# Performance work log

Measured on AMD Instinct MI355X. Metric: run time of the kernel, lower is better.

## Reference

```python
import jax, jax.numpy as jnp
import numpy as np


def _rope_cos_sin(seq_len, dim, dtype):
    inv_freq = 1.0 / (10000.0 ** (jnp.arange(0, dim, 2, dtype=jnp.float32) / dim))
    t = jnp.arange(seq_len, dtype=jnp.float32)
    freqs = jnp.einsum('i,j->ij', t, inv_freq)          # [S, dim/2]
    emb = jnp.concatenate([freqs, freqs], axis=-1)       # [S, dim]
    return emb.astype(dtype).__class__ and (jnp.cos(emb).astype(dtype), jnp.sin(emb).astype(dtype))


def _apply_rope(x, cos, sin):
    half = x.shape[-1] // 2
    rot = jnp.concatenate([-x[..., half:], x[..., :half]], axis=-1)
    return x * cos + rot * sin


def setup_inputs() -> dict:
    key = jax.random.key(0)
    kq, kk, kv = jax.random.split(key, 3)
    B, S, D = 8, 4096, 128
    Q = jax.random.normal(kq, (B, S, D), dtype=jnp.float32)
    K = jax.random.normal(kk, (B, S, D), dtype=jnp.float32)
    V = jax.random.normal(kv, (B, S, D), dtype=jnp.float32)
    return {"Q": Q, "K": K, "V": V}


def reference(Q, K, V):
    B, S, D = Q.shape
    cos, sin = _rope_cos_sin(S, D, Q.dtype)              # [S, D] each
    Qr = _apply_rope(Q, cos, sin)
    Kr = _apply_rope(K, cos, sin)
    energy = jnp.einsum('bsd,btd->bst', Qr, Kr)          # [B, S, S]
    causal = jnp.tril(jnp.ones((S, S), dtype=bool))
    energy = jnp.where(causal, energy, jnp.zeros((), dtype=energy.dtype))
    return jnp.einsum('bst,btd->bsd', energy, V)
```

## Files before the change

### kernel.cpp

```cpp
#include <hip/hip_runtime.h>
#include <hip/hip_bf16.h>

#define B_ 8
#define S_ 4096
#define D_ 128
#define C_ 256
#define NC 16

typedef __attribute__((ext_vector_type(8))) short bf16x8;
typedef __attribute__((ext_vector_type(4))) float f32x4;
typedef __attribute__((ext_vector_type(4))) unsigned u32x4;

static __device__ __forceinline__ unsigned short f2bf(float x) {
    unsigned u = __float_as_uint(x);
    u += 0x7fffu + ((u >> 16) & 1u);
    return (unsigned short)(u >> 16);
}

typedef const __attribute__((address_space(1))) unsigned int* gas_ptr;
typedef __attribute__((address_space(3))) unsigned int* las_ptr;
static __device__ __forceinline__ void load_lds16(const unsigned short* g, unsigned short* l) {
    __builtin_amdgcn_global_load_lds((gas_ptr)(const void*)g, (las_ptr)(void*)l, 16, 0, 0);
}

#define WAIT_VMCNT_8 do { asm volatile("s_waitcnt vmcnt(8)" ::: "memory"); \
                          __builtin_amdgcn_sched_barrier(0); } while (0)
#define WAIT_VMCNT_0 do { asm volatile("s_waitcnt vmcnt(0)" ::: "memory"); \
                          __builtin_amdgcn_sched_barrier(0); } while (0)
#define BARRIER      do { __builtin_amdgcn_s_barrier(); \
                          __builtin_amdgcn_sched_barrier(0); } while (0)

__global__ __launch_bounds__(512, 2) void fusedA(const float* __restrict__ K,
                                                 const float* __restrict__ V,
                                                 unsigned short* __restrict__ Kr,
                                                 unsigned short* __restrict__ Vt,
                                                 float* __restrict__ P1) {
    __shared__ unsigned short Klds[128 * 128];
    __shared__ unsigned short Vlds[128 * 128];

    const int b    = blockIdx.x >> 5;
    const int c    = (blockIdx.x >> 1) & 15;
    const int half = blockIdx.x & 1;
    const int tid  = threadIdx.x;
    const int t0   = c * C_ + half * 128;

    #pragma unroll
    for (int it = 0; it < 4; ++it) {
        int e  = it * 512 + tid;
        int tl = e >> 4;
        int d0 = (e & 15) * 4;
        size_t gbase = ((size_t)(b * S_ + t0 + tl)) * D_;
        float ka[4], kb[4], va[4], vb[4];
        *(float4*)ka = *(const float4*)(K + gbase + d0);
        *(float4*)kb = *(const float4*)(K + gbase + d0 + 64);
        *(float4*)va = *(const float4*)(V + gbase + d0);
        *(float4*)vb = *(const float4*)(V + gbase + d0 + 64);
        unsigned short kl[4], kh[4];
        #pragma unroll
        for (int jj = 0; jj < 4; ++jj) {
            float invf = exp2f(-0.20762050f * (float)(d0 + jj));
            float ang = (float)(t0 + tl) * invf;
            float sn, cs;
            __sincosf(ang, &sn, &cs);
            kl[jj] = f2bf(ka[jj] * cs - kb[jj] * sn);
            kh[jj] = f2bf(kb[jj] * cs + ka[jj] * sn);
        }
        *reinterpret_cast<ushort4*>(Kr + gbase + d0)      = ushort4{kl[0], kl[1], kl[2], kl[3]};
        *reinterpret_cast<ushort4*>(Kr + gbase + d0 + 64) = ushort4{kh[0], kh[1], kh[2], kh[3]};
        int cc = tl >> 3, tr = tl & 7;
        #pragma unroll
        for (int jj = 0; jj < 4; ++jj) {
            int dA = d0 + jj, dB = d0 + 64 + jj;
            Klds[dA * 128 + ((cc ^ (dA & 15)) * 8) + tr] = kl[jj];
            Klds[dB * 128 + ((cc ^ (dB & 15)) * 8) + tr] = kh[jj];
            Vlds[dA * 128 + ((cc ^ (dA & 15)) * 8) + tr] = f2bf(va[jj]);
            Vlds[dB * 128 + ((cc ^ (dB & 15)) * 8) + tr] = f2bf(vb[jj]);
        }
    }
    __syncthreads();

    #pragma unroll
    for (int it = 0; it < 4; ++it) {
        int e = it * 512 + tid;
        int d = e >> 4;
        int cc = e & 15;
        const bf16x8 v8 = *reinterpret_cast<const bf16x8*>(
            &Vlds[d * 128 + ((cc ^ (d & 15)) * 8)]);
        *reinterpret_cast<bf16x8*>(
            Vt + ((size_t)(b * D_ + d)) * S_ + t0 + cc * 8) = v8;
    }

    const int w = tid >> 6, l = tid & 63, g = l >> 4, n = l & 15;
    f32x4 acc[8];
    #pragma unroll
    for (int dc = 0; dc < 8; ++dc) acc[dc] = f32x4{0.f, 0.f, 0.f, 0.f};

    #pragma unroll
    for (int ki = 0; ki < 4; ++ki) {
        const int arow = 16 * w + n;
        const bf16x8 a = *reinterpret_cast<const bf16x8*>(
            &Vlds[arow * 128 + (((4 * ki + g) ^ n) * 8)]);
        #pragma unroll
        for (int dc = 0; dc < 8; ++dc) {
            int row = dc * 16 + n;
            const bf16x8 bb = *reinterpret_cast<const bf16x8*>(
                &Klds[row * 128 + (((4 * ki + g) ^ n) * 8)]);
            acc[dc] = __builtin_amdgcn_mfma_f32_16x16x32_bf16(a, bb, acc[dc], 0, 0, 0);
        }
    }

    float* out = P1 + (size_t)((b * NC + c) * 2 + half) * D_ * D_;
    #pragma unroll
    for (int dc = 0; dc < 8; ++dc)
        #pragma unroll
        for (int rr = 0; rr < 4; ++rr)
            out[(size_t)(16 * w + 4 * g + rr) * D_ + dc * 16 + n] = acc[dc][rr];
}

__global__ __launch_bounds__(256) void prefix(const float* __restrict__ P1,
                                              unsigned short* __restrict__ Hhi) {
    int gid = blockIdx.x * 256 + threadIdx.x;
    int d  = gid & 127;
    int dp = (gid >> 7) & 127;
    int b  = gid >> 14;
    float run = 0.f;
    #pragma unroll
    for (int c = 0; c < NC; ++c) {
        size_t hidx = ((size_t)(b * NC + c) * D_ + dp) * D_ + d;
        Hhi[hidx] = f2bf(run);
        size_t p = ((size_t)((b * NC + c) * 2) * D_ + dp) * D_ + d;
        run += P1[p];
        run += P1[p + (size_t)D_ * D_];
    }
}

__global__ __launch_bounds__(256, 2) void pass2(const float* __restrict__ Q,
                                                const unsigned short* __restrict__ Kr,
                                                const unsigned short* __restrict__ Vt,
                                                const unsigned short* __restrict__ Hhi,
                                                float* __restrict__ Out) {
    __shared__ unsigned short Kb[2][64 * 128];
    __shared__ unsigned short Vb[2][128 * 64];

    const int bid = blockIdx.x;
    const int ppmap[4] = {3, 2, 0, 1};
    const int pp = ppmap[bid >> 7];
    const int r2 = bid & 127;
    const int b  = r2 & 7;
    const int c  = r2 >> 3;
    const int qg = c * 4 + pp;
    const int c4 = c * 4;

    const int tid = threadIdx.x;
    const int wv = tid >> 6;
    const int l  = tid & 63;
    const int g  = l >> 4;
    const int n  = l & 15;

    bf16x8 qf[4];
    {
        const int s = qg * 64 + wv * 16 + n;
        const float* qp = Q + ((size_t)(b * S_ + s)) * D_ + 8 * g;
        float qv[4][8];
        #pragma unroll
        for (int ks = 0; ks < 4; ++ks) {
            *reinterpret_cast<float4*>(&qv[ks][0]) =
                *reinterpret_cast<const float4*>(qp + 32 * ks);
            *reinterpret_cast<float4*>(&qv[ks][4]) =
                *reinterpret_cast<const float4*>(qp + 32 * ks + 4);
        }
        unsigned short qb[4][8];
        #pragma unroll
        for (int hf = 0; hf < 2; ++hf)
            #pragma unroll
            for (int j = 0; j < 8; ++j) {
                int dm = 32 * hf + 8 * g + j;
                float invf = exp2f(-0.20762050f * (float)dm);
                float ang = (float)s * invf;
                float sn, cs;
                __sincosf(ang, &sn, &cs);
                qb[hf][j]     = f2bf(qv[hf][j] * cs - qv[hf + 2][j] * sn);
                qb[hf + 2][j] = f2bf(qv[hf + 2][j] * cs + qv[hf][j] * sn);
            }
        #pragma unroll
        for (int ks = 0; ks < 4; ++ks) {
            bf16x8 f;
            #pragma unroll
            for (int j = 0; j < 8; ++j) f[j] = (short)qb[ks][j];
            qf[ks] = f;
        }
    }

    auto stage = [&](int bufs, int tg) {
        const unsigned short* kbase = Kr + ((size_t)(b * S_ + tg * 64)) * D_;
        #pragma unroll
        for (int i = 0; i < 4; ++i) {
            int ci = i * 256 + tid;
            int t = ci >> 4, cc = ci & 15;
            load_lds16(kbase + t * D_ + ((cc ^ (t & 15)) * 8), &Kb[bufs][ci * 8]);
        }
        const unsigned short* vbase = Vt + (size_t)b * D_ * S_ + (size_t)tg * 64;
        #pragma unroll
        for (int i = 0; i < 4; ++i) {
            int ci = i * 256 + tid;
            int d = ci >> 3, cc = ci & 7;
            load_lds16(vbase + (size_t)d * S_ + ((cc ^ (d & 7)) * 8), &Vb[bufs][ci * 8]);
        }
    };

    f32x4 o[8];
    #pragma unroll
    for (int df = 0; df < 8; ++df) o[df] = f32x4{0.f, 0.f, 0.f, 0.f};

    stage(0, c4);
    if (pp >= 1) stage(1, c4 + 1);

    {
        const unsigned short* hbase = Hhi + (size_t)(b * NC + c) * D_ * D_;
        #pragma unroll
        for (int ks = 0; ks < 4; ++ks) {
            #pragma unroll
            for (int df = 0; df < 8; ++df) {
                const bf16x8 hh = *reinterpret_cast<const bf16x8*>(
                    hbase + (size_t)(df * 16 + n) * D_ + 32 * ks + 8 * g);
                o[df] = __builtin_amdgcn_mfma_f32_16x16x32_bf16(qf[ks], hh, o[df], 0, 0, 0);
            }
        }
    }

    for (int kt = 0; kt <= pp; ++kt) {
        if (kt < pp) { WAIT_VMCNT_8; }
        else         { WAIT_VMCNT_0; }
        BARRIER;

        const int bufc = kt & 1;

        f32x4 e[4];
        #pragma unroll
        for (int tf = 0; tf < 4; ++tf) e[tf] = f32x4{0.f, 0.f, 0.f, 0.f};
        __builtin_amdgcn_s_setprio(1);
        #pragma unroll
        for (int tf = 0; tf < 4; ++tf) {
            #pragma unroll
            for (int ks = 0; ks < 4; ++ks) {
                const bf16x8 kf = *reinterpret_cast<const bf16x8*>(
                    &Kb[bufc][(tf * 16 + n) * 128 + (((4 * ks + g) ^ n) * 8)]);
                e[tf] = __builtin_amdgcn_mfma_f32_16x16x32_bf16(kf, qf[ks], e[tf], 0, 0, 0);
            }
        }
        __builtin_amdgcn_s_setprio(0);

        if (kt == pp) {
            int s_glob = qg * 64 + wv * 16 + n;
            #pragma unroll
            for (int tf = 0; tf < 4; ++tf)
                #pragma unroll
                for (int rr = 0; rr < 4; ++rr) {
                    int t_glob = (c4 + kt) * 64 + tf * 16 + 4 * g + rr;
                    if (t_glob > s_glob) e[tf][rr] = 0.f;
                }
        }

        bf16x8 pf[2];
        {
            unsigned u0[4], u1[4];
            #pragma unroll
            for (int tf = 0; tf < 4; ++tf) {
                asm("v_cvt_pk_bf16_f32 %0, %1, %2"
                    : "=v"(u0[tf]) : "v"(e[tf][0]), "v"(e[tf][1]));
                asm("v_cvt_pk_bf16_f32 %0, %1, %2"
                    : "=v"(u1[tf]) : "v"(e[tf][2]), "v"(e[tf][3]));
            }
            #pragma unroll
            for (int ks = 0; ks < 2; ++ks) {
                unsigned a0 = u0[2 * ks], a1 = u0[2 * ks + 1];
                unsigned b0 = u1[2 * ks], b1 = u1[2 * ks + 1];
                asm("v_permlane32_swap_b32 %0, %1" : "+v"(a0), "+v"(a1));
                asm("v_permlane32_swap_b32 %0, %1" : "+v"(b0), "+v"(b1));
                asm("v_permlane16_swap_b32 %0, %1" : "+v"(a0), "+v"(a1));
                asm("v_permlane16_swap_b32 %0, %1" : "+v"(b0), "+v"(b1));
                pf[ks] = __builtin_bit_cast(bf16x8, u32x4{a0, b0, a1, b1});
            }
        }

        __builtin_amdgcn_s_setprio(1);
        #pragma unroll
        for (int df = 0; df < 8; ++df) {
            #pragma unroll
            for (int ks = 0; ks < 2; ++ks) {
                const bf16x8 vf = *reinterpret_cast<const bf16x8*>(
                    &Vb[bufc][(df * 16 + n) * 64 + (((4 * ks + g) ^ (n & 7)) * 8)]);
                o[df] = __builtin_amdgcn_mfma_f32_16x16x32_bf16(pf[ks], vf, o[df], 0, 0, 0);
            }
        }
        __builtin_amdgcn_s_setprio(0);

        BARRIER;

        if (kt + 2 <= pp) stage(bufc, c4 + kt + 2);
    }

    #pragma unroll
    for (int df = 0; df < 8; ++df)
        #pragma unroll
        for (int rr = 0; rr < 4; ++rr) {
            int srow = qg * 64 + wv * 16 + 4 * g + rr;
            Out[((size_t)(b * S_ + srow)) * D_ + df * 16 + n] = o[df][rr];
        }
}

extern "C" void kernel_launch(void* const* d_in, const int* in_sizes, int n_in,
                              void* d_out, int out_size, void* d_ws, size_t ws_size,
                              hipStream_t stream) {
    const float* Q = (const float*)d_in[0];
    const float* K = (const float*)d_in[1];
    const float* V = (const float*)d_in[2];

    const size_t NE = (size_t)B_ * S_ * D_;
    unsigned short* Kr = (unsigned short*)d_ws;
    unsigned short* Vt = Kr + NE;
    float*          P1 = (float*)(Vt + NE);
    unsigned short* Hhi = (unsigned short*)(P1 + (size_t)B_ * NC * 2 * D_ * D_);

    fusedA<<<256, 512, 0, stream>>>(K, V, Kr, Vt, P1);
    prefix<<<512, 256, 0, stream>>>(P1, Hhi);
    pass2 <<<512, 256, 0, stream>>>(Q, Kr, Vt, Hhi, (float*)d_out);
}
```

Before: 40.74 us.

## Store partial KV products in bf16 and merge pass2 into 512-thread blocks

fusedA now writes its per-chunk K^T V partial products as bf16 instead of fp32, which halves the write and read traffic for the prefix kernel at the cost of extra rounding error. pass2 is restructured so each 512-thread block handles 128 query rows (8 waves), sharing the staged K/V tiles across twice as many waves and halving the grid. The staging loads are split over more threads and the wait count is adjusted to match. The causal mask is now applied on every tile iteration rather than only the last one, adding some ALU work, and each half-block now walks through 2 or 4 K tiles.

```diff
diff --git a/kernel.cpp b/kernel.cpp
--- a/kernel.cpp
+++ b/kernel.cpp
@@ -16,6 +16,9 @@
     u += 0x7fffu + ((u >> 16) & 1u);
     return (unsigned short)(u >> 16);
 }
+static __device__ __forceinline__ float bf2f(unsigned short h) {
+    return __uint_as_float(((unsigned)h) << 16);
+}
 
 typedef const __attribute__((address_space(1))) unsigned int* gas_ptr;
 typedef __attribute__((address_space(3))) unsigned int* las_ptr;
@@ -23,7 +26,7 @@
     __builtin_amdgcn_global_load_lds((gas_ptr)(const void*)g, (las_ptr)(void*)l, 16, 0, 0);
 }
 
-#define WAIT_VMCNT_8 do { asm volatile("s_waitcnt vmcnt(8)" ::: "memory"); \
+#define WAIT_VMCNT_4 do { asm volatile("s_waitcnt vmcnt(4)" ::: "memory"); \
                           __builtin_amdgcn_sched_barrier(0); } while (0)
 #define WAIT_VMCNT_0 do { asm volatile("s_waitcnt vmcnt(0)" ::: "memory"); \
                           __builtin_amdgcn_sched_barrier(0); } while (0)
@@ -34,7 +37,7 @@
                                                  const float* __restrict__ V,
                                                  unsigned short* __restrict__ Kr,
                                                  unsigned short* __restrict__ Vt,
-                                                 float* __restrict__ P1) {
+                                                 unsigned short* __restrict__ P1h) {
     __shared__ unsigned short Klds[128 * 128];
     __shared__ unsigned short Vlds[128 * 128];
 
@@ -109,15 +112,15 @@
         }
     }
 
-    float* out = P1 + (size_t)((b * NC + c) * 2 + half) * D_ * D_;
+    unsigned short* out = P1h + (size_t)((b * NC + c) * 2 + half) * D_ * D_;
     #pragma unroll
     for (int dc = 0; dc < 8; ++dc)
         #pragma unroll
         for (int rr = 0; rr < 4; ++rr)
-            out[(size_t)(16 * w + 4 * g + rr) * D_ + dc * 16 + n] = acc[dc][rr];
-}
-
-__global__ __launch_bounds__(256) void prefix(const float* __restrict__ P1,
+            out[(size_t)(16 * w + 4 * g + rr) * D_ + dc * 16 + n] = f2bf(acc[dc][rr]);
+}
+
+__global__ __launch_bounds__(256) void prefix(const unsigned short* __restrict__ P1h,
                                               unsigned short* __restrict__ Hhi) {
     int gid = blockIdx.x * 256 + threadIdx.x;
     int d  = gid & 127;
@@ -129,12 +132,12 @@
         size_t hidx = ((size_t)(b * NC + c) * D_ + dp) * D_ + d;
         Hhi[hidx] = f2bf(run);
         size_t p = ((size_t)((b * NC + c) * 2) * D_ + dp) * D_ + d;
-        run += P1[p];
-        run += P1[p + (size_t)D_ * D_];
-    }
-}
-
-__global__ __launch_bounds__(256, 2) void pass2(const float* __restrict__ Q,
+        run += bf2f(P1h[p]);
+        run += bf2f(P1h[p + (size_t)D_ * D_]);
+    }
+}
+
+__global__ __launch_bounds__(512, 4) void pass2(const float* __restrict__ Q,
                                                 const unsigned short* __restrict__ Kr,
                                                 const unsigned short* __restrict__ Vt,
                                                 const unsigned short* __restrict__ Hhi,
@@ -142,24 +145,24 @@
     __shared__ unsigned short Kb[2][64 * 128];
     __shared__ unsigned short Vb[2][128 * 64];
 
-    const int bid = blockIdx.x;
-    const int ppmap[4] = {3, 2, 0, 1};
-    const int pp = ppmap[bid >> 7];
-    const int r2 = bid & 127;
-    const int b  = r2 & 7;
-    const int c  = r2 >> 3;
-    const int qg = c * 4 + pp;
-    const int c4 = c * 4;
+    const int bid  = blockIdx.x;
+    const int half = (bid < 128) ? 1 : 0;
+    const int r2   = bid & 127;
+    const int b    = r2 & 7;
+    const int c    = r2 >> 3;
+    const int c4   = c * 4;
+    const int ppmax = 2 * half + 1;
 
     const int tid = threadIdx.x;
     const int wv = tid >> 6;
     const int l  = tid & 63;
     const int g  = l >> 4;
     const int n  = l & 15;
+    const int srow0 = c * 256 + half * 128 + wv * 16;
 
     bf16x8 qf[4];
     {
-        const int s = qg * 64 + wv * 16 + n;
+        const int s = srow0 + n;
         const float* qp = Q + ((size_t)(b * S_ + s)) * D_ + 8 * g;
         float qv[4][8];
         #pragma unroll
@@ -194,15 +197,15 @@
     auto stage = [&](int bufs, int tg) {
         const unsigned short* kbase = Kr + ((size_t)(b * S_ + tg * 64)) * D_;
         #pragma unroll
-        for (int i = 0; i < 4; ++i) {
-            int ci = i * 256 + tid;
+        for (int i = 0; i < 2; ++i) {
+            int ci = i * 512 + tid;
             int t = ci >> 4, cc = ci & 15;
             load_lds16(kbase + t * D_ + ((cc ^ (t & 15)) * 8), &Kb[bufs][ci * 8]);
         }
         const unsigned short* vbase = Vt + (size_t)b * D_ * S_ + (size_t)tg * 64;
         #pragma unroll
-        for (int i = 0; i < 4; ++i) {
-            int ci = i * 256 + tid;
+        for (int i = 0; i < 2; ++i) {
+            int ci = i * 512 + tid;
             int d = ci >> 3, cc = ci & 7;
             load_lds16(vbase + (size_t)d * S_ + ((cc ^ (d & 7)) * 8), &Vb[bufs][ci * 8]);
         }
@@ -213,7 +216,7 @@
     for (int df = 0; df < 8; ++df) o[df] = f32x4{0.f, 0.f, 0.f, 0.f};
 
     stage(0, c4);
-    if (pp >= 1) stage(1, c4 + 1);
+    stage(1, c4 + 1);
 
     {
         const unsigned short* hbase = Hhi + (size_t)(b * NC + c) * D_ * D_;
@@ -228,9 +231,9 @@
         }
     }
 
-    for (int kt = 0; kt <= pp; ++kt) {
-        if (kt < pp) { WAIT_VMCNT_8; }
-        else         { WAIT_VMCNT_0; }
+    for (int kt = 0; kt <= ppmax; ++kt) {
+        if (kt < ppmax) { WAIT_VMCNT_4; }
+        else            { WAIT_VMCNT_0; }
         BARRIER;
 
         const int bufc = kt & 1;
@@ -250,8 +253,8 @@
         }
         __builtin_amdgcn_s_setprio(0);
 
-        if (kt == pp) {
-            int s_glob = qg * 64 + wv * 16 + n;
+        {
+            int s_glob = srow0 + n;
             #pragma unroll
             for (int tf = 0; tf < 4; ++tf)
                 #pragma unroll
@@ -297,14 +300,14 @@
 
         BARRIER;
 
-        if (kt + 2 <= pp) stage(bufc, c4 + kt + 2);
+        if (kt + 2 <= ppmax) stage(bufc, c4 + kt + 2);
     }
 
     #pragma unroll
     for (int df = 0; df < 8; ++df)
         #pragma unroll
         for (int rr = 0; rr < 4; ++rr) {
-            int srow = qg * 64 + wv * 16 + 4 * g + rr;
+            int srow = srow0 + 4 * g + rr;
             Out[((size_t)(b * S_ + srow)) * D_ + df * 16 + n] = o[df][rr];
         }
 }
@@ -317,12 +320,12 @@
     const float* V = (const float*)d_in[2];
 
     const size_t NE = (size_t)B_ * S_ * D_;
-    unsigned short* Kr = (unsigned short*)d_ws;
-    unsigned short* Vt = Kr + NE;
-    float*          P1 = (float*)(Vt + NE);
-    unsigned short* Hhi = (unsigned short*)(P1 + (size_t)B_ * NC * 2 * D_ * D_);
-
-    fusedA<<<256, 512, 0, stream>>>(K, V, Kr, Vt, P1);
-    prefix<<<512, 256, 0, stream>>>(P1, Hhi);
-    pass2 <<<512, 256, 0, stream>>>(Q, Kr, Vt, Hhi, (float*)d_out);
-}
+    unsigned short* Kr  = (unsigned short*)d_ws;
+    unsigned short* Vt  = Kr + NE;
+    unsigned short* P1h = Vt + NE;
+    unsigned short* Hhi = P1h + (size_t)B_ * NC * 2 * D_ * D_;
+
+    fusedA<<<256, 512, 0, stream>>>(K, V, Kr, Vt, P1h);
+    prefix<<<512, 256, 0, stream>>>(P1h, Hhi);
+    pass2 <<<256, 512, 0, stream>>>(Q, Kr, Vt, Hhi, (float*)d_out);
+}
```

Measured after the change: 39.77 us. 2.4% less time.
